# Performance work log

Hardware: AMD Instinct MI355X
Metric: run time of the kernel (lower is better)

The kernel has to match this reference:

```python
import jax, jax.numpy as jnp
import numpy as np

T = 4096      # sentence length
V = 50257     # vocab size
E = 1024      # embedding dim
H = 512       # hidden per direction (hidden_dim // 2)
NT = 32       # tagset size


def setup_inputs() -> dict:
    key = jax.random.key(0)
    ks = jax.random.split(key, 12)
    s = 0.02
    return {
        "sentence": jax.random.randint(ks[0], (T,), 0, V, dtype=jnp.int32),
        "emb": jax.random.normal(ks[1], (V, E), jnp.float32) * s,
        "W_ih_f": jax.random.normal(ks[2], (3 * H, E), jnp.float32) * s,
        "W_hh_f": jax.random.normal(ks[3], (3 * H, H), jnp.float32) * s,
        "b_ih_f": jax.random.normal(ks[4], (3 * H,), jnp.float32) * s,
        "b_hh_f": jax.random.normal(ks[5], (3 * H,), jnp.float32) * s,
        "W_ih_b": jax.random.normal(ks[6], (3 * H, E), jnp.float32) * s,
        "W_hh_b": jax.random.normal(ks[7], (3 * H, H), jnp.float32) * s,
        "b_ih_b": jax.random.normal(ks[8], (3 * H,), jnp.float32) * s,
        "b_hh_b": jax.random.normal(ks[9], (3 * H,), jnp.float32) * s,
        "W_out": jax.random.normal(ks[10], (NT, E), jnp.float32) * s,
    }


def _gru_dir(x, W_ih, W_hh, b_ih, b_hh):
    """Run a single-direction GRU over x [T, E] -> hidden states [T, H].
    PyTorch GRU gate math: r,z,n order; h' = (1-z)*n + z*h; h0 = 0."""
    gi = x @ W_ih.T + b_ih  # [T, 3H] input projections, one big GEMM

    def step(h, gi_t):
        gh = h @ W_hh.T + b_hh            # [3H]
        ir, iz, inn = jnp.split(gi_t, 3)
        hr, hz, hn = jnp.split(gh, 3)
        r = jax.nn.sigmoid(ir + hr)
        z = jax.nn.sigmoid(iz + hz)
        n = jnp.tanh(inn + r * hn)
        h_new = (1.0 - z) * n + z * h
        return h_new, h_new

    h0 = jnp.zeros((W_hh.shape[1],), x.dtype)
    _, hs = jax.lax.scan(step, h0, gi)
    return hs  # [T, H]


def reference(sentence, emb, W_ih_f, W_hh_f, b_ih_f, b_hh_f,
              W_ih_b, W_hh_b, b_ih_b, b_hh_b, W_out):
    x = emb[sentence]  # [T, E] embedding lookup
    h_fwd = _gru_dir(x, W_ih_f, W_hh_f, b_ih_f, b_hh_f)            # [T, H]
    h_bwd = _gru_dir(x[::-1], W_ih_b, W_hh_b, b_ih_b, b_hh_b)[::-1]  # [T, H]
    h = jnp.concatenate([h_fwd, h_bwd], axis=-1)  # [T, 2H]
    return h @ W_out.T  # [T, NT] tag scores (no bias)
```

## Files before the change

### kernel.cpp

```cpp
#include <hip/hip_runtime.h>

#define T_LEN 4096
#define E_DIM 1024
#define H_DIM 512
#define NT_DIM 32
#define NG 3072
#define G_DIR 64
#define OPW 8

typedef __attribute__((ext_vector_type(8))) short bf16x8;
typedef __attribute__((ext_vector_type(4))) float f32x4;
typedef unsigned long long ull;

__device__ inline unsigned short f2bf(float f) {
    unsigned int u = __float_as_uint(f);
    unsigned int r = (u + 0x7fffu + ((u >> 16) & 1u)) >> 16;
    return (unsigned short)r;
}
__device__ inline float bf2f(unsigned short u) {
    return __uint_as_float(((unsigned int)u) << 16);
}
__device__ inline ull packhs(float v, unsigned tag) {
    return (ull)__float_as_uint(v) | ((ull)tag << 32);
}

__global__ void embed_cast(const int* __restrict__ sent, const float* __restrict__ emb,
                           unsigned short* __restrict__ xb) {
    int t = blockIdx.x;
    int row = sent[t];
    const float4* src = (const float4*)(emb + (size_t)row * E_DIM);
    ushort4* dst = (ushort4*)(xb + (size_t)t * E_DIM);
    float4 v = src[threadIdx.x];
    ushort4 o;
    o.x = f2bf(v.x); o.y = f2bf(v.y); o.z = f2bf(v.z); o.w = f2bf(v.w);
    dst[threadIdx.x] = o;
}

__global__ void wcast(const float* __restrict__ wf, const float* __restrict__ wb_,
                      unsigned short* __restrict__ w) {
    int r = blockIdx.x;
    const float* src = (r < 1536) ? (wf + (size_t)r * E_DIM) : (wb_ + (size_t)(r - 1536) * E_DIM);
    const float4* s4 = (const float4*)src;
    ushort4* dst = (ushort4*)(w + (size_t)r * E_DIM);
    float4 v = s4[threadIdx.x];
    ushort4 o;
    o.x = f2bf(v.x); o.y = f2bf(v.y); o.z = f2bf(v.z); o.w = f2bf(v.w);
    dst[threadIdx.x] = o;
}

#define LDST 40
__global__ __launch_bounds__(256) void gi_gemm(const unsigned short* __restrict__ xb,
                                               const unsigned short* __restrict__ wb,
                                               const float* __restrict__ bihf,
                                               const float* __restrict__ bihb,
                                               unsigned short* __restrict__ gi) {
    __shared__ __align__(16) unsigned short As[64 * LDST];
    __shared__ __align__(16) unsigned short Bs[64 * LDST];
    int tile_m = (blockIdx.x % 64) * 64;
    int tile_n = (blockIdx.x / 64) * 64;
    int tid = threadIdx.x;
    int lane = tid & 63, wv = tid >> 6;
    int quad = lane >> 4, r15 = lane & 15;
    int srow = tid >> 2, sseg = tid & 3;

    f32x4 acc[4] = {};
    for (int kb = 0; kb < E_DIM; kb += 32) {
        uint4 a = *(const uint4*)(xb + (size_t)(tile_m + srow) * E_DIM + kb + sseg * 8);
        uint4 b = *(const uint4*)(wb + (size_t)(tile_n + srow) * E_DIM + kb + sseg * 8);
        *(uint4*)&As[srow * LDST + sseg * 8] = a;
        *(uint4*)&Bs[srow * LDST + sseg * 8] = b;
        __syncthreads();
        bf16x8 af = *(bf16x8*)&As[(wv * 16 + r15) * LDST + quad * 8];
#pragma unroll
        for (int nt = 0; nt < 4; nt++) {
            bf16x8 bf = *(bf16x8*)&Bs[(nt * 16 + r15) * LDST + quad * 8];
            acc[nt] = __builtin_amdgcn_mfma_f32_16x16x32_bf16(af, bf, acc[nt], 0, 0, 0);
        }
        __syncthreads();
    }
#pragma unroll
    for (int nt = 0; nt < 4; nt++) {
        int gn = tile_n + nt * 16 + r15;
        float bias = (gn < 1536) ? bihf[gn] : bihb[gn - 1536];
#pragma unroll
        for (int rg = 0; rg < 4; rg++) {
            int gm = tile_m + wv * 16 + quad * 4 + rg;
            gi[(size_t)gm * NG + gn] = f2bf(acc[nt][rg] + bias);
        }
    }
}

__global__ __launch_bounds__(512) void gru_rec(
    const float* __restrict__ whhf, const float* __restrict__ bhhf,
    const float* __restrict__ whhb, const float* __restrict__ bhhb,
    const unsigned short* __restrict__ gi, ull* __restrict__ hxf, ull* __restrict__ hxb) {
    int wgid = blockIdx.x;
    int dir = wgid >> 6;
    int g = wgid & 63;
    const float* whh = dir ? whhb : whhf;
    const float* bhh = dir ? bhhb : bhhf;
    ull* hx = dir ? hxb : hxf;

    int tid = threadIdx.x;
    int kp = tid & 7;
    int q = tid >> 3;
    int kg = g * OPW + kp;
    int wave = tid >> 6;
    int lane = tid & 63;

    float4 wr[2], wz[2], wn[2];
    {
        const float4* pr_ = (const float4*)(whh + (size_t)kg * H_DIM + q * 8);
        const float4* pz_ = (const float4*)(whh + (size_t)(kg + 512) * H_DIM + q * 8);
        const float4* pn_ = (const float4*)(whh + (size_t)(kg + 1024) * H_DIM + q * 8);
        wr[0] = pr_[0]; wr[1] = pr_[1];
        wz[0] = pz_[0]; wz[1] = pz_[1];
        wn[0] = pn_[0]; wn[1] = pn_[1];
    }
    float bias_r = 0.f, bias_z = 0.f, bias_n = 0.f, h_own = 0.f;
    int kg0 = g * OPW + tid;
    if (tid < OPW) {
        bias_r = bhh[kg0]; bias_z = bhh[kg0 + 512]; bias_n = bhh[kg0 + 1024];
    }

    __shared__ float hsh[512];
    __shared__ float part[3][8][OPW];

    for (int s = 0; s < T_LEN; s++) {
        int row = dir ? (T_LEN - 1 - s) : s;
        float gir = 0.f, giz = 0.f, gin = 0.f;
        if (tid < OPW) {
            const unsigned short* gp = gi + (size_t)row * NG + dir * 1536 + kg0;
            gir = bf2f(gp[0]); giz = bf2f(gp[512]); gin = bf2f(gp[1024]);
        }
        float hv = 0.f;
        if (s > 0) {
            int prow = dir ? (T_LEN - s) : (s - 1);
            const ull* slot = hx + (size_t)prow * H_DIM + tid;
            ull p;
            do {
                p = __hip_atomic_load(slot, __ATOMIC_RELAXED, __HIP_MEMORY_SCOPE_AGENT);
            } while ((unsigned)(p >> 32) != (unsigned)s);
            hv = __uint_as_float((unsigned)p);
        }
        hsh[tid] = hv;
        __syncthreads();

        float4 h0 = *(const float4*)&hsh[q * 8];
        float4 h1 = *(const float4*)&hsh[q * 8 + 4];
        float pr, pz, pn;
        pr  = wr[0].x * h0.x + wr[0].y * h0.y + wr[0].z * h0.z + wr[0].w * h0.w
            + wr[1].x * h1.x + wr[1].y * h1.y + wr[1].z * h1.z + wr[1].w * h1.w;
        pz  = wz[0].x * h0.x + wz[0].y * h0.y + wz[0].z * h0.z + wz[0].w * h0.w
            + wz[1].x * h1.x + wz[1].y * h1.y + wz[1].z * h1.z + wz[1].w * h1.w;
        pn  = wn[0].x * h0.x + wn[0].y * h0.y + wn[0].z * h0.z + wn[0].w * h0.w
            + wn[1].x * h1.x + wn[1].y * h1.y + wn[1].z * h1.z + wn[1].w * h1.w;
        pr += __shfl_xor(pr, 8);  pz += __shfl_xor(pz, 8);  pn += __shfl_xor(pn, 8);
        pr += __shfl_xor(pr, 16); pz += __shfl_xor(pz, 16); pn += __shfl_xor(pn, 16);
        pr += __shfl_xor(pr, 32); pz += __shfl_xor(pz, 32); pn += __shfl_xor(pn, 32);
        if (lane < OPW) {
            part[0][wave][lane] = pr; part[1][wave][lane] = pz; part[2][wave][lane] = pn;
        }
        __syncthreads();

        if (tid < OPW) {
            float sr = bias_r, sz = bias_z, sn = bias_n;
#pragma unroll
            for (int w = 0; w < 8; w++) {
                sr += part[0][w][tid]; sz += part[1][w][tid]; sn += part[2][w][tid];
            }
            float rr = 1.f / (1.f + __expf(-(gir + sr)));
            float zz = 1.f / (1.f + __expf(-(giz + sz)));
            float a = gin + rr * sn;
            a = fminf(20.f, fmaxf(-20.f, a));
            float e = __expf(-2.f * a);
            float nn = (1.f - e) / (1.f + e);
            float hnew = (1.f - zz) * nn + zz * h_own;
            h_own = hnew;
            __hip_atomic_store(hx + (size_t)row * H_DIM + kg0, packhs(hnew, (unsigned)(s + 1)),
                               __ATOMIC_RELAXED, __HIP_MEMORY_SCOPE_AGENT);
        }
    }
}

__global__ __launch_bounds__(256) void out_gemm(const ull* __restrict__ hxf,
                                                const ull* __restrict__ hxb,
                                                const float* __restrict__ wout,
                                                float* __restrict__ out) {
    __shared__ __align__(16) float ls[8][1028];
    int t0 = blockIdx.x * 8;
    int tid = threadIdx.x;
#pragma unroll
    for (int i = 0; i < 8; i++) {
        int col = tid * 4;
        const ull* src = (col < 512) ? (hxf + (size_t)(t0 + i) * H_DIM + col)
                                     : (hxb + (size_t)(t0 + i) * H_DIM + (col - 512));
        ull s0 = src[0], s1 = src[1], s2 = src[2], s3 = src[3];
        ls[i][col + 0] = __uint_as_float((unsigned)s0);
        ls[i][col + 1] = __uint_as_float((unsigned)s1);
        ls[i][col + 2] = __uint_as_float((unsigned)s2);
        ls[i][col + 3] = __uint_as_float((unsigned)s3);
    }
    __syncthreads();
    int r8 = tid >> 5, gg = tid & 31;
    const float4* wp = (const float4*)(wout + (size_t)gg * 1024);
    float sum = 0.f;
#pragma unroll 8
    for (int j = 0; j < 256; j++) {
        float4 w = wp[j];
        float4 h = *(const float4*)&ls[r8][j * 4];
        sum += w.x * h.x + w.y * h.y + w.z * h.z + w.w * h.w;
    }
    out[(size_t)(t0 + r8) * NT_DIM + gg] = sum;
}

extern "C" void kernel_launch(void* const* d_in, const int* in_sizes, int n_in,
                              void* d_out, int out_size, void* d_ws, size_t ws_size,
                              hipStream_t stream) {
    const int*   sent = (const int*)d_in[0];
    const float* emb  = (const float*)d_in[1];
    const float* wihf = (const float*)d_in[2];
    const float* whhf = (const float*)d_in[3];
    const float* bihf = (const float*)d_in[4];
    const float* bhhf = (const float*)d_in[5];
    const float* wihb = (const float*)d_in[6];
    const float* whhb = (const float*)d_in[7];
    const float* bihb = (const float*)d_in[8];
    const float* bhhb = (const float*)d_in[9];
    const float* wout = (const float*)d_in[10];

    char* ws = (char*)d_ws;
    unsigned short* gi  = (unsigned short*)(ws);
    unsigned short* xb  = (unsigned short*)(ws + 25165824);
    unsigned short* wb  = (unsigned short*)(ws + 33554432);
    ull*            hxf = (ull*)(ws + 39845888);
    ull*            hxb = (ull*)(ws + 56623104);
    float*          out = (float*)d_out;

    embed_cast<<<T_LEN, 256, 0, stream>>>(sent, emb, xb);
    wcast<<<NG, 256, 0, stream>>>(wihf, wihb, wb);
    gi_gemm<<<64 * 48, 256, 0, stream>>>(xb, wb, bihf, bihb, gi);
    gru_rec<<<2 * G_DIR, 512, 0, stream>>>(whhf, bhhf, whhb, bhhb, gi, hxf, hxb);
    out_gemm<<<T_LEN / 8, 256, 0, stream>>>(hxf, hxb, wout, out);
}
```

Before: 7.053 ms.

## Use 16 wider GRU workgroups per direction with one barrier per step

```diff
diff --git a/kernel.cpp b/kernel.cpp
--- a/kernel.cpp
+++ b/kernel.cpp
@@ -5,8 +5,8 @@
 #define H_DIM 512
 #define NT_DIM 32
 #define NG 3072
-#define G_DIR 64
-#define OPW 8
+#define G_DIR 16
+#define OPW 32
 
 typedef __attribute__((ext_vector_type(8))) short bf16x8;
 typedef __attribute__((ext_vector_type(4))) float f32x4;
@@ -90,85 +90,94 @@
     }
 }
 
-__global__ __launch_bounds__(512) void gru_rec(
+__global__ __launch_bounds__(512, 1) void gru_rec(
     const float* __restrict__ whhf, const float* __restrict__ bhhf,
     const float* __restrict__ whhb, const float* __restrict__ bhhb,
     const unsigned short* __restrict__ gi, ull* __restrict__ hxf, ull* __restrict__ hxb) {
     int wgid = blockIdx.x;
-    int dir = wgid >> 6;
-    int g = wgid & 63;
+    int dir = wgid >> 4;
+    int g = wgid & 15;
     const float* whh = dir ? whhb : whhf;
     const float* bhh = dir ? bhhb : bhhf;
     ull* hx = dir ? hxb : hxf;
 
     int tid = threadIdx.x;
-    int kp = tid & 7;
-    int q = tid >> 3;
+    int lane = tid & 63;
+    int wave = tid >> 6;
+    int kp = lane & 31;
+    int qh = lane >> 5;
+    int q = wave * 2 + qh;
     int kg = g * OPW + kp;
-    int wave = tid >> 6;
-    int lane = tid & 63;
-
-    float4 wr[2], wz[2], wn[2];
+
+    float4 wr[8], wz[8], wn[8];
     {
-        const float4* pr_ = (const float4*)(whh + (size_t)kg * H_DIM + q * 8);
-        const float4* pz_ = (const float4*)(whh + (size_t)(kg + 512) * H_DIM + q * 8);
-        const float4* pn_ = (const float4*)(whh + (size_t)(kg + 1024) * H_DIM + q * 8);
-        wr[0] = pr_[0]; wr[1] = pr_[1];
-        wz[0] = pz_[0]; wz[1] = pz_[1];
-        wn[0] = pn_[0]; wn[1] = pn_[1];
+        const float4* pr_ = (const float4*)(whh + (size_t)kg * H_DIM + q * 32);
+        const float4* pz_ = (const float4*)(whh + (size_t)(kg + 512) * H_DIM + q * 32);
+        const float4* pn_ = (const float4*)(whh + (size_t)(kg + 1024) * H_DIM + q * 32);
+#pragma unroll
+        for (int i = 0; i < 8; i++) { wr[i] = pr_[i]; wz[i] = pz_[i]; wn[i] = pn_[i]; }
     }
     float bias_r = 0.f, bias_z = 0.f, bias_n = 0.f, h_own = 0.f;
-    int kg0 = g * OPW + tid;
-    if (tid < OPW) {
-        bias_r = bhh[kg0]; bias_z = bhh[kg0 + 512]; bias_n = bhh[kg0 + 1024];
+    int kgo = g * OPW + lane;
+    if (wave == 0 && lane < OPW) {
+        bias_r = bhh[kgo]; bias_z = bhh[kgo + 512]; bias_n = bhh[kgo + 1024];
     }
 
     __shared__ float hsh[512];
-    __shared__ float part[3][8][OPW];
+    __shared__ float part[2][3][8][OPW];
+
+    unsigned short gu0 = 0, gu1 = 0, gu2 = 0;
 
     for (int s = 0; s < T_LEN; s++) {
         int row = dir ? (T_LEN - 1 - s) : s;
-        float gir = 0.f, giz = 0.f, gin = 0.f;
-        if (tid < OPW) {
-            const unsigned short* gp = gi + (size_t)row * NG + dir * 1536 + kg0;
-            gir = bf2f(gp[0]); giz = bf2f(gp[512]); gin = bf2f(gp[1024]);
+        if (wave == 0 && lane < OPW) {
+            const unsigned short* gp = gi + (size_t)row * NG + dir * 1536 + kgo;
+            gu0 = gp[0]; gu1 = gp[512]; gu2 = gp[1024];
         }
         float hv = 0.f;
         if (s > 0) {
             int prow = dir ? (T_LEN - s) : (s - 1);
-            const ull* slot = hx + (size_t)prow * H_DIM + tid;
-            ull p;
-            do {
-                p = __hip_atomic_load(slot, __ATOMIC_RELAXED, __HIP_MEMORY_SCOPE_AGENT);
-            } while ((unsigned)(p >> 32) != (unsigned)s);
-            hv = __uint_as_float((unsigned)p);
-        }
-        hsh[tid] = hv;
+            const ull* slot = hx + (size_t)prow * H_DIM + wave * 64 + lane;
+            ull v = 0; bool ok = false;
+            for (;;) {
+                if (!ok) {
+                    v = __hip_atomic_load(slot, __ATOMIC_RELAXED, __HIP_MEMORY_SCOPE_AGENT);
+                    ok = ((unsigned)(v >> 32) == (unsigned)s);
+                }
+                if (__all(ok)) break;
+            }
+            hv = __uint_as_float((unsigned)v);
+        }
+        hsh[wave * 64 + lane] = hv;
+        const float4* hp = (const float4*)&hsh[wave * 64 + qh * 32];
+        float pr = 0.f, pz = 0.f, pn = 0.f;
+#pragma unroll
+        for (int i = 0; i < 8; i++) {
+            float4 h4 = hp[i];
+            pr += wr[i].x * h4.x + wr[i].y * h4.y + wr[i].z * h4.z + wr[i].w * h4.w;
+            pz += wz[i].x * h4.x + wz[i].y * h4.y + wz[i].z * h4.z + wz[i].w * h4.w;
+            pn += wn[i].x * h4.x + wn[i].y * h4.y + wn[i].z * h4.z + wn[i].w * h4.w;
+        }
+        pr += __shfl_xor(pr, 32);
+        pz += __shfl_xor(pz, 32);
+        pn += __shfl_xor(pn, 32);
+        int par = s & 1;
+        if (lane < OPW) {
+            part[par][0][wave][lane] = pr;
+            part[par][1][wave][lane] = pz;
+            part[par][2][wave][lane] = pn;
+        }
         __syncthreads();
 
-        float4 h0 = *(const float4*)&hsh[q * 8];
-        float4 h1 = *(const float4*)&hsh[q * 8 + 4];
-        float pr, pz, pn;
-        pr  = wr[0].x * h0.x + wr[0].y * h0.y + wr[0].z * h0.z + wr[0].w * h0.w
-            + wr[1].x * h1.x + wr[1].y * h1.y + wr[1].z * h1.z + wr[1].w * h1.w;
-        pz  = wz[0].x * h0.x + wz[0].y * h0.y + wz[0].z * h0.z + wz[0].w * h0.w
-            + wz[1].x * h1.x + wz[1].y * h1.y + wz[1].z * h1.z + wz[1].w * h1.w;
-        pn  = wn[0].x * h0.x + wn[0].y * h0.y + wn[0].z * h0.z + wn[0].w * h0.w
-            + wn[1].x * h1.x + wn[1].y * h1.y + wn[1].z * h1.z + wn[1].w * h1.w;
-        pr += __shfl_xor(pr, 8);  pz += __shfl_xor(pz, 8);  pn += __shfl_xor(pn, 8);
-        pr += __shfl_xor(pr, 16); pz += __shfl_xor(pz, 16); pn += __shfl_xor(pn, 16);
-        pr += __shfl_xor(pr, 32); pz += __shfl_xor(pz, 32); pn += __shfl_xor(pn, 32);
-        if (lane < OPW) {
-            part[0][wave][lane] = pr; part[1][wave][lane] = pz; part[2][wave][lane] = pn;
-        }
-        __syncthreads();
-
-        if (tid < OPW) {
+        if (wave == 0 && lane < OPW) {
             float sr = bias_r, sz = bias_z, sn = bias_n;
 #pragma unroll
             for (int w = 0; w < 8; w++) {
-                sr += part[0][w][tid]; sz += part[1][w][tid]; sn += part[2][w][tid];
+                sr += part[par][0][w][lane];
+                sz += part[par][1][w][lane];
+                sn += part[par][2][w][lane];
             }
+            float gir = bf2f(gu0), giz = bf2f(gu1), gin = bf2f(gu2);
             float rr = 1.f / (1.f + __expf(-(gir + sr)));
             float zz = 1.f / (1.f + __expf(-(giz + sz)));
             float a = gin + rr * sn;
@@ -177,7 +186,7 @@
             float nn = (1.f - e) / (1.f + e);
             float hnew = (1.f - zz) * nn + zz * h_own;
             h_own = hnew;
-            __hip_atomic_store(hx + (size_t)row * H_DIM + kg0, packhs(hnew, (unsigned)(s + 1)),
+            __hip_atomic_store(hx + (size_t)row * H_DIM + kgo, packhs(hnew, (unsigned)(s + 1)),
                                __ATOMIC_RELAXED, __HIP_MEMORY_SCOPE_AGENT);
         }
     }
```

After: 6.969 ms. No clear change (-1.2%).
